# Performance work log

Hardware: AMD Instinct MI355X
Metric: run time of the kernel (lower is better)

## Reference

```python
import jax, jax.numpy as jnp
import numpy as np

V = 20000          # vocab size ('ALL')
E = 512            # embedding_dim
H = 1024           # rnn_hidden_size
LD = 256           # latent_dim
NL = 2             # num_rnn_layers_dec (hidden_factor = 2, unidirectional)
B = 32
S = 256
PAD = 0
CUT0 = 30          # cutoffs = [30, 100, 1000], div_value = 4.0
TAIL_SPECS = [(30, 100, 256), (100, 1000, 64), (1000, V, 16)]  # (low, high, proj_dim)


def setup_inputs() -> dict:
    key = jax.random.key(0)
    ks = jax.random.split(key, 24)
    w = lambda k, shp: (0.02 * jax.random.normal(k, shp)).astype(jnp.float32)

    z = jax.random.normal(ks[0], (B, LD), dtype=jnp.float32)
    emb = w(ks[1], (V, E))
    l2h_w = w(ks[2], (NL * H, LD))
    l2h_b = jnp.zeros((NL * H,), jnp.float32)
    # RNN layer 0 (input E) and layer 1 (input H)
    rnn0_wih = w(ks[3], (H, E)); rnn0_whh = w(ks[4], (H, H))
    rnn0_bih = jnp.zeros((H,), jnp.float32); rnn0_bhh = jnp.zeros((H,), jnp.float32)
    rnn1_wih = w(ks[5], (H, H)); rnn1_whh = w(ks[6], (H, H))
    rnn1_bih = jnp.zeros((H,), jnp.float32); rnn1_bhh = jnp.zeros((H,), jnp.float32)
    # adaptive softmax: head = 30 shortlist + 3 cluster logits
    head_w = w(ks[7], (CUT0 + 3, H))
    tail_p0 = w(ks[8], (256, H));  tail_w0 = w(ks[9], (70, 256))
    tail_p1 = w(ks[10], (64, H));  tail_w1 = w(ks[11], (900, 64))
    tail_p2 = w(ks[12], (16, H));  tail_w2 = w(ks[13], (V - 1000, 16))

    length = jax.random.randint(ks[14], (B,), 32, S + 1)
    pos = jnp.arange(S)[None, :]
    mask = pos < length[:, None]
    inp_seq = jax.random.randint(ks[15], (B, S), 4, V)
    inp_seq = jnp.where(mask, inp_seq, PAD)
    target_seq = jax.random.randint(ks[16], (B, S), 4, V)
    target_seq = jnp.where(mask, target_seq, PAD)

    return dict(z=z, emb=emb, l2h_w=l2h_w, l2h_b=l2h_b,
                rnn0_wih=rnn0_wih, rnn0_whh=rnn0_whh, rnn0_bih=rnn0_bih, rnn0_bhh=rnn0_bhh,
                rnn1_wih=rnn1_wih, rnn1_whh=rnn1_whh, rnn1_bih=rnn1_bih, rnn1_bhh=rnn1_bhh,
                head_w=head_w, tail_p0=tail_p0, tail_w0=tail_w0, tail_p1=tail_p1,
                tail_w1=tail_w1, tail_p2=tail_p2, tail_w2=tail_w2,
                inp_seq=inp_seq, target_seq=target_seq, length=length)


def _rnn_layer(x, h0, wih, whh, bih, bhh):
    # x: [B,S,D], h0: [B,H] -> [B,S,H]  (tanh vanilla RNN)
    def step(h, xt):
        h = jnp.tanh(xt @ wih.T + bih + h @ whh.T + bhh)
        return h, h
    _, ys = jax.lax.scan(step, h0, jnp.swapaxes(x, 0, 1))
    return jnp.swapaxes(ys, 0, 1)


def _adaptive_log_prob(x, head_w, tails):
    # x: [N,H] -> full log-probs [N,V] (AdaptiveLogSoftmaxWithLoss.log_prob)
    head_lp = jax.nn.log_softmax(x @ head_w.T, axis=-1)  # [N, 33]
    parts = [head_lp[:, :CUT0]]
    for i, (p, w) in enumerate(tails):
        clp = jax.nn.log_softmax((x @ p.T) @ w.T, axis=-1)
        parts.append(clp + head_lp[:, CUT0 + i][:, None])
    return jnp.concatenate(parts, axis=1)


def reference(z, emb, l2h_w, l2h_b,
              rnn0_wih, rnn0_whh, rnn0_bih, rnn0_bhh,
              rnn1_wih, rnn1_whh, rnn1_bih, rnn1_bhh,
              head_w, tail_p0, tail_w0, tail_p1, tail_w1, tail_p2, tail_w2,
              inp_seq, target_seq, length):
    # sort inputs by descending length (hidden is NOT sorted, as in the original)
    sorted_idx = jnp.argsort(-length)
    x = emb[inp_seq[sorted_idx]]                         # [B,S,E]
    hid = z @ l2h_w.T + l2h_b                            # [B, 2H]
    hidden = hid.reshape(NL, B, H)                       # torch .view(hidden_factor, B, H)
    h1 = _rnn_layer(x, hidden[0], rnn0_wih, rnn0_whh, rnn0_bih, rnn0_bhh)
    h2 = _rnn_layer(h1, hidden[1], rnn1_wih, rnn1_whh, rnn1_bih, rnn1_bhh)
    rev = jnp.argsort(sorted_idx)
    out = h2[rev].reshape(-1, H)                         # [N,H]
    tgt = target_seq.reshape(-1)                         # [N]
    lp = _adaptive_log_prob(out, head_w,
                            [(tail_p0, tail_w0), (tail_p1, tail_w1), (tail_p2, tail_w2)])
    nll = -jnp.take_along_axis(lp, tgt[:, None], axis=1)[:, 0]
    nll = jnp.where(tgt == PAD, 0.0, nll)
    return jnp.sum(nll)
```

## Files before the change

### kernel.cpp

```cpp
#include <hip/hip_runtime.h>
#include <hip/hip_bf16.h>
#include <math.h>

#define BB 32
#define SS 256
#define EE 512
#define HH 1024
#define LDM 256
#define NROW (BB*SS)

typedef __attribute__((ext_vector_type(8))) short bf16x8;
typedef __attribute__((ext_vector_type(4))) float f32x4;
typedef unsigned long long u64;

static __device__ inline unsigned short f2bf(float f){
  unsigned u = __float_as_uint(f);
  unsigned r = (u + 0x7fffu + ((u >> 16) & 1u)) >> 16;
  return (unsigned short)r;
}
static __device__ inline unsigned short f2bf_fast(float f){
  return (unsigned short)((__float_as_uint(f) + 0x8000u) >> 16);
}
static __device__ inline bf16x8 cvt8(float4 x, float4 y){
  union { ushort s[8]; bf16x8 v; } t;
  t.s[0]=f2bf_fast(x.x); t.s[1]=f2bf_fast(x.y); t.s[2]=f2bf_fast(x.z); t.s[3]=f2bf_fast(x.w);
  t.s[4]=f2bf_fast(y.x); t.s[5]=f2bf_fast(y.y); t.s[6]=f2bf_fast(y.z); t.s[7]=f2bf_fast(y.w);
  return t.v;
}
static __device__ inline unsigned packbf(float a, float b){
  return (unsigned)f2bf(a) | ((unsigned)f2bf(b) << 16);
}

static __device__ inline float ftanh(float x){
  float e = __expf(2.f*x);
  return 1.f - 2.f/(e + 1.f);
}

#define GLD(dst, p) asm volatile("global_load_dwordx4 %0, %1, off sc0 sc1" \
                                 : "=v"(dst) : "v"(p) : "memory")

static __device__ inline bf16x8 asbf(f32x4 x){
  union { f32x4 f; bf16x8 b; } u; u.f = x; return u.b;
}

__global__ void k_sort(const int* __restrict__ length, int* __restrict__ sorted_idx){
  int b = threadIdx.x;
  if (b >= BB) return;
  int lb = length[b];
  int r = 0;
  for (int o = 0; o < BB; ++o){
    int lo = length[o];
    if (lo > lb || (lo == lb && o < b)) ++r;
  }
  sorted_idx[r] = b;
}

__global__ void k_maps(const int* __restrict__ sorted_idx,
                       const int* __restrict__ inp_seq, const int* __restrict__ tgt_seq,
                       int* __restrict__ tokmap, int* __restrict__ tgtmap){
  int bs = blockIdx.x; int t = threadIdx.x;
  int b = sorted_idx[bs];
  tokmap[bs*SS + t] = inp_seq[b*SS + t];
  tgtmap[bs*SS + t] = tgt_seq[b*SS + t];
}

__global__ __launch_bounds__(256) void k_hid(const float* __restrict__ z,
        const float* __restrict__ w, const float* __restrict__ bias,
        ushort* __restrict__ hb0){
  int id = blockIdx.x*256 + threadIdx.x;
  int b = id >> 11, c = id & 2047;
  const float4* zr = (const float4*)(z + b*LDM);
  const float4* wr = (const float4*)(w + (size_t)c*LDM);
  float a0=0,a1=0,a2=0,a3=0;
  #pragma unroll 4
  for (int k=0;k<LDM/4;k++){ float4 zz=zr[k], ww=wr[k];
    a0+=zz.x*ww.x; a1+=zz.y*ww.y; a2+=zz.z*ww.z; a3+=zz.w*ww.w; }
  float val = a0+a1+a2+a3 + bias[c];
  int layer = id >> 15, bp = (id >> 10) & 31, j = id & 1023;
  hb0[(layer<<15) + ((j>>3)<<8) + (bp<<3) + (j&7)] = f2bf(val);
}

__global__ __launch_bounds__(256) void k_wcat(
    const float* __restrict__ head_w, const float* __restrict__ p0,
    const float* __restrict__ p1, const float* __restrict__ p2,
    float* __restrict__ wcat){
  int row = blockIdx.x; int t = threadIdx.x;
  float4* dst = (float4*)(wcat + (size_t)row*HH);
  const float* src;
  if      (row < 33)  src = head_w + (size_t)row*HH;
  else if (row < 289) src = p0 + (size_t)(row-33)*HH;
  else if (row < 353) src = p1 + (size_t)(row-289)*HH;
  else if (row < 369) src = p2 + (size_t)(row-353)*HH;
  else { dst[t] = make_float4(0.f,0.f,0.f,0.f); return; }
  dst[t] = ((const float4*)src)[t];
}

__global__ __launch_bounds__(256) void k_bin(
    const int* __restrict__ tgtmap, int* __restrict__ cnt,
    int* __restrict__ l0, int* __restrict__ l1, int* __restrict__ l2)
{
  int row = blockIdx.x*256 + threadIdx.x;
  int tgt = tgtmap[row];
  int ci = (tgt == 0) ? -1 : (tgt >= 1000) ? 2 : (tgt >= 100) ? 1 : (tgt >= 30) ? 0 : -1;
  int lane = threadIdx.x & 63;
  #pragma unroll
  for (int c = 0; c < 3; ++c){
    unsigned long long mask = __ballot(ci == c);
    int nc = __popcll(mask);
    int base = 0;
    if (lane == 0 && nc) base = atomicAdd(&cnt[c], nc);
    base = __shfl(base, 0);
    if (ci == c){
      int pos = __popcll(mask & ((1ull << lane) - 1ull));
      int* lst = (c == 0) ? l0 : (c == 1) ? l1 : l2;
      lst[base + pos] = row;
    }
  }
}

__global__ __launch_bounds__(256) void k_gemm_bf16(
    const float* __restrict__ A, int lda, const int* __restrict__ rowmap, int abf16,
    const float* __restrict__ Bm,
    const float* __restrict__ bias0, const float* __restrict__ bias1,
    float* __restrict__ C, int M, int N, int K)
{
  __shared__ ushort As[128*72];
  __shared__ ushort Bs[128*72];
  const int nt = blockIdx.x * 128, mt = blockIdx.y * 128;
  const int tid = threadIdx.x;
  const int wv = tid >> 6, ln = tid & 63;
  const int wm = wv & 1, wn = wv >> 1;
  const int lc = ln & 15, quad = ln >> 4;
  f32x4 acc[4][4] = {{{0.f,0.f,0.f,0.f}}};

  for (int s = 0; s < K; s += 64){
    __syncthreads();
    #pragma unroll
    for (int cc = 0; cc < 4; ++cc){
      int ch = tid*4 + cc;
      int r = ch >> 3, c = ch & 7;
      int ar = mt + r;
      if (abf16){
        const ushort* ap = (const ushort*)A + (size_t)ar*lda + s + c*8;
        *(bf16x8*)&As[r*72 + c*8] = *(const bf16x8*)ap;
      } else {
        const float* ap = A + (size_t)(rowmap ? rowmap[ar] : ar)*lda + s + c*8;
        float4 x = *(const float4*)ap, y = *(const float4*)(ap+4);
        *(bf16x8*)&As[r*72 + c*8] = cvt8(x, y);
      }
      int br = nt + r; if (br >= N) br = N - 1;
      const float* bp = Bm + (size_t)br*K + s + c*8;
      float4 bx = *(const float4*)bp, by = *(const float4*)(bp+4);
      *(bf16x8*)&Bs[r*72 + c*8] = cvt8(bx, by);
    }
    __syncthreads();
    #pragma unroll
    for (int kq = 0; kq < 2; ++kq){
      int cq = kq*4 + quad;
      bf16x8 af[4], bfv[4];
      #pragma unroll
      for (int i=0;i<4;i++) af[i]  = *(const bf16x8*)&As[(wm*64 + i*16 + lc)*72 + cq*8];
      #pragma unroll
      for (int j=0;j<4;j++) bfv[j] = *(const bf16x8*)&Bs[(wn*64 + j*16 + lc)*72 + cq*8];
      #pragma unroll
      for (int i=0;i<4;i++)
        #pragma unroll
        for (int j=0;j<4;j++)
          acc[i][j] = __builtin_amdgcn_mfma_f32_16x16x32_bf16(af[i], bfv[j], acc[i][j], 0, 0, 0);
    }
  }
  #pragma unroll
  for (int j=0;j<4;j++){
    int col = nt + wn*64 + j*16 + lc;
    if (col < N){
      float badd = (bias0 ? bias0[col] : 0.f) + (bias1 ? bias1[col] : 0.f);
      #pragma unroll
      for (int i=0;i<4;i++){
        int row = mt + wm*64 + i*16 + quad*4;
        #pragma unroll
        for (int r=0;r<4;r++)
          C[(size_t)(row+r)*N + col] = acc[i][j][r] + badd;
      }
    }
  }
}

__global__ __launch_bounds__(256, 1) void k_rnn_split(
    const float* __restrict__ pre0, ushort* __restrict__ h2out,
    const float* __restrict__ w0hh, const float* __restrict__ w1ih,
    const float* __restrict__ w1hh,
    const float* __restrict__ b1ih, const float* __restrict__ b1hh,
    const ushort* __restrict__ hb0, ushort* __restrict__ hx, int* flags)
{
  __shared__ ushort w0F[16384], wiF[16384], whF[16384];
  __shared__ float red[2176];
  const int wg  = blockIdx.x;
  const int tid = threadIdx.x;
  const bool roleL2 = wg >= 64;
  const int cw  = roleL2 ? wg - 64 : wg;
  const int j0  = cw * 16;
  int* myctr = flags + (roleL2 ? 256 : 0) + (cw & 7) * 32;

  for (int c = tid; c < 4096; c += 256){
    int rr = c >> 8, cc = (c & 255) * 4;
    int dst = ((cc >> 3)*16 + rr)*8 + (cc & 7);
    size_t srow = (size_t)(j0 + rr)*HH + cc;
    float4 w4; uint2 p;
    if (!roleL2){
      w4 = *(const float4*)&w0hh[srow];
      p.x = packbf(w4.x, w4.y); p.y = packbf(w4.z, w4.w);
      *(uint2*)&w0F[dst] = p;
    } else {
      w4 = *(const float4*)&w1ih[srow];
      p.x = packbf(w4.x, w4.y); p.y = packbf(w4.z, w4.w);
      *(uint2*)&wiF[dst] = p;
      w4 = *(const float4*)&w1hh[srow];
      p.x = packbf(w4.x, w4.y); p.y = packbf(w4.z, w4.w);
      *(uint2*)&whF[dst] = p;
    }
  }
  const int lane = tid & 63, wv = tid >> 6;
  const int col = lane & 15, quad = lane >> 4;
  const int ob = tid >> 3, oj = (tid << 1) & 15;
  const int ro = ob*17 + oj;
  const int k = j0 + oj;
  const unsigned off = ((unsigned)(k >> 3) << 7) + ((unsigned)ob << 2) + ((unsigned)(k & 7) >> 1);
  ushort* h1buf = hx;
  ushort* h2buf = hx + 3*32768;

  if (!roleL2){
    float2 pre = *(const float2*)&pre0[((size_t)ob*SS + 0)*HH + j0 + oj];
    __syncthreads();
    for (int t = 0; t < SS; ++t){
      const u64* s1 = (const u64*)(t == 0 ? hb0 : h1buf + ((t+2)%3)*32768);
      f32x4 a0r[8], a1r[8];
      #pragma unroll
      for (int ks = 0; ks < 8; ++ks){
        int kb = wv*32 + ks*4 + quad;
        const u64* p = s1 + (kb << 6) + (col << 1);
        GLD(a0r[ks], p);
        GLD(a1r[ks], p + 32);
      }
      asm volatile("s_waitcnt vmcnt(0)" ::: "memory");
      __builtin_amdgcn_sched_barrier(0);

      f32x4 acc0 = {0.f,0.f,0.f,0.f}, acc1 = {0.f,0.f,0.f,0.f};
      #pragma unroll
      for (int ks = 0; ks < 8; ++ks){
        int kb = wv*32 + ks*4 + quad;
        bf16x8 b0 = *(const bf16x8*)&w0F[(kb*16 + col)*8];
        acc0 = __builtin_amdgcn_mfma_f32_16x16x32_bf16(asbf(a0r[ks]), b0, acc0, 0, 0, 0);
        acc1 = __builtin_amdgcn_mfma_f32_16x16x32_bf16(asbf(a1r[ks]), b0, acc1, 0, 0, 0);
      }
      #pragma unroll
      for (int q = 0; q < 4; ++q){
        red[wv*544 + (quad*4 + q)*17 + col]      = acc0[q];
        red[wv*544 + (16 + quad*4 + q)*17 + col] = acc1[q];
      }
      __syncthreads();
      float s0 = red[ro]   + red[544 + ro]   + red[1088 + ro]   + red[1632 + ro];
      float s1v= red[ro+1] + red[544 + ro+1] + red[1088 + ro+1] + red[1632 + ro+1];
      unsigned pk = packbf(ftanh(pre.x + s0), ftanh(pre.y + s1v));
      __hip_atomic_store((unsigned*)(h1buf + (t%3)*32768) + off, pk,
                         __ATOMIC_RELAXED, __HIP_MEMORY_SCOPE_AGENT);
      asm volatile("s_waitcnt vmcnt(0)" ::: "memory");
      __syncthreads();
      if (tid == 0)
        __hip_atomic_fetch_add(myctr, 1, __ATOMIC_RELAXED, __HIP_MEMORY_SCOPE_AGENT);

      int tn = (t + 1 < SS) ? t + 1 : SS - 1;
      pre = *(const float2*)&pre0[((size_t)ob*SS + tn)*HH + j0 + oj];

      if (t < SS - 1 && tid < 16){
        int tv = (tid < 8) ? 8*(t+1) : 8*(t-1);
        const int* fp = flags + ((tid < 8) ? 0 : 256) + (tid & 7)*32;
        if (tv > 0)
          while (__hip_atomic_load(fp, __ATOMIC_RELAXED, __HIP_MEMORY_SCOPE_AGENT) < tv) {}
      }
      __syncthreads();
    }
  } else {
    float2 pre2;
    pre2.x = b1ih[j0+oj]   + b1hh[j0+oj];
    pre2.y = b1ih[j0+oj+1] + b1hh[j0+oj+1];
    __syncthreads();
    if (tid < 8){
      while (__hip_atomic_load(flags + tid*32, __ATOMIC_RELAXED,
                               __HIP_MEMORY_SCOPE_AGENT) < 8) {}
    }
    __syncthreads();
    for (int s = 0; s < SS; ++s){
      const u64* sa = (const u64*)(h1buf + (s%3)*32768);
      const u64* sc = (const u64*)(s == 0 ? hb0 + 32768
                                          : h2buf + ((s+1)&1)*32768);
      f32x4 a0r[8], a1r[8], c0r[8], c1r[8];
      #pragma unroll
      for (int ks = 0; ks < 8; ++ks){
        int kb = wv*32 + ks*4 + quad;
        const u64* p = sa + (kb << 6) + (col << 1);
        GLD(a0r[ks], p);
        GLD(a1r[ks], p + 32);
      }
      #pragma unroll
      for (int ks = 0; ks < 8; ++ks){
        int kb = wv*32 + ks*4 + quad;
        const u64* p = sc + (kb << 6) + (col << 1);
        GLD(c0r[ks], p);
        GLD(c1r[ks], p + 32);
      }
      asm volatile("s_waitcnt vmcnt(0)" ::: "memory");
      __builtin_amdgcn_sched_barrier(0);

      f32x4 acc0 = {0.f,0.f,0.f,0.f}, acc1 = {0.f,0.f,0.f,0.f};
      #pragma unroll
      for (int ks = 0; ks < 8; ++ks){
        int kb = wv*32 + ks*4 + quad;
        bf16x8 bi = *(const bf16x8*)&wiF[(kb*16 + col)*8];
        acc0 = __builtin_amdgcn_mfma_f32_16x16x32_bf16(asbf(a0r[ks]), bi, acc0, 0, 0, 0);
        acc1 = __builtin_amdgcn_mfma_f32_16x16x32_bf16(asbf(a1r[ks]), bi, acc1, 0, 0, 0);
        bf16x8 bh = *(const bf16x8*)&whF[(kb*16 + col)*8];
        acc0 = __builtin_amdgcn_mfma_f32_16x16x32_bf16(asbf(c0r[ks]), bh, acc0, 0, 0, 0);
        acc1 = __builtin_amdgcn_mfma_f32_16x16x32_bf16(asbf(c1r[ks]), bh, acc1, 0, 0, 0);
      }
      #pragma unroll
      for (int q = 0; q < 4; ++q){
        red[wv*544 + (quad*4 + q)*17 + col]      = acc0[q];
        red[wv*544 + (16 + quad*4 + q)*17 + col] = acc1[q];
      }
      __syncthreads();
      float s2v = red[ro]   + red[544 + ro]   + red[1088 + ro]   + red[1632 + ro];
      float s3v = red[ro+1] + red[544 + ro+1] + red[1088 + ro+1] + red[1632 + ro+1];
      unsigned pk2 = packbf(ftanh(pre2.x + s2v), ftanh(pre2.y + s3v));
      __hip_atomic_store((unsigned*)(h2buf + (s&1)*32768) + off, pk2,
                         __ATOMIC_RELAXED, __HIP_MEMORY_SCOPE_AGENT);
      asm volatile("s_waitcnt vmcnt(0)" ::: "memory");
      __syncthreads();
      if (tid == 0)
        __hip_atomic_fetch_add(myctr, 1, __ATOMIC_RELAXED, __HIP_MEMORY_SCOPE_AGENT);

      *((unsigned*)h2out + (((size_t)ob*SS + s)*HH + j0 + oj) / 2) = pk2;

      if (s < SS - 1 && tid < 16){
        int tv = (tid < 8) ? 8*(s+2) : 8*(s+1);
        const int* fp = flags + ((tid < 8) ? 0 : 256) + (tid & 7)*32;
        while (__hip_atomic_load(fp, __ATOMIC_RELAXED, __HIP_MEMORY_SCOPE_AGENT) < tv) {}
      }
      __syncthreads();
    }
  }
}

__global__ __launch_bounds__(256) void k_cluster(
    const float* __restrict__ combo, int off, int ld, int Kp,
    const float* __restrict__ W, int Nc,
    const int* __restrict__ rowlist, const int* __restrict__ cntp, int ci,
    float* __restrict__ stats)
{
  __shared__ float ps[4][4][256];
  int lane = threadIdx.x & 63;
  int wvl  = threadIdx.x >> 6;
  int n0 = (blockIdx.x*4 + wvl) * 4;
  int count = cntp[ci];
  int rows[4];
  #pragma unroll
  for (int r=0;r<4;r++){
    rows[r] = (n0 + r < count) ? rowlist[n0 + r] : -1;
    if (rows[r] >= 0)
      for (int k=lane;k<Kp;k+=64)
        ps[wvl][r][k] = combo[(size_t)rows[r]*ld + off + k];
  }
  __syncthreads();
  if (rows[0] < 0) return;

  float mx[4], sm[4];
  #pragma unroll
  for (int r=0;r<4;r++){ mx[r]=-1e30f; sm[r]=0.f; }
  for (int n=lane; n<Nc; n+=64){
    const float* wr = W + (size_t)n*Kp;
    float l[4]={0.f,0.f,0.f,0.f};
    for (int k=0;k<Kp;k+=4){
      float4 w4 = *(const float4*)(wr+k);
      #pragma unroll
      for (int r=0;r<4;r++){
        l[r] += w4.x*ps[wvl][r][k] + w4.y*ps[wvl][r][k+1]
              + w4.z*ps[wvl][r][k+2] + w4.w*ps[wvl][r][k+3];
      }
    }
    #pragma unroll
    for (int r=0;r<4;r++){
      float nm = fmaxf(mx[r], l[r]);
      sm[r] = sm[r]*__expf(mx[r]-nm) + __expf(l[r]-nm);
      mx[r] = nm;
    }
  }
  #pragma unroll
  for (int r=0;r<4;r++){
    for (int off2=32; off2; off2>>=1){
      float om = __shfl_down(mx[r], off2);
      float os = __shfl_down(sm[r], off2);
      float nm = fmaxf(mx[r], om);
      sm[r] = sm[r]*__expf(mx[r]-nm) + os*__expf(om-nm);
      mx[r] = nm;
    }
    if (lane==0 && rows[r] >= 0){
      stats[(size_t)rows[r]*6 + ci*2 + 0] = mx[r];
      stats[(size_t)rows[r]*6 + ci*2 + 1] = sm[r];
    }
  }
}

__global__ __launch_bounds__(256) void k_tlogit(
    const int* __restrict__ tgtmap, const float* __restrict__ combo,
    const float* __restrict__ w0, const float* __restrict__ w1, const float* __restrict__ w2,
    float* __restrict__ tlogit)
{
  int lane = threadIdx.x & 63;
  int row = (blockIdx.x * 256 + threadIdx.x) >> 6;
  int tgt = tgtmap[row];
  float acc = 0.f;
  const float* pr = nullptr; const float* wr = nullptr; int Kp = 0;
  const float* crow = combo + (size_t)row*384;
  if      (tgt >= 1000){ pr = crow + 353; wr = w2 + (size_t)(tgt-1000)*16;  Kp=16;  }
  else if (tgt >= 100) { pr = crow + 289; wr = w1 + (size_t)(tgt-100)*64;   Kp=64;  }
  else if (tgt >= 30)  { pr = crow + 33;  wr = w0 + (size_t)(tgt-30)*256;   Kp=256; }
  for (int k=lane; k<Kp; k+=64) acc += pr[k]*wr[k];
  for (int off=32; off; off>>=1) acc += __shfl_down(acc, off);
  if (lane==0) tlogit[row] = acc;
}

__global__ __launch_bounds__(256) void k_final(
    const float* __restrict__ combo, const float* __restrict__ stats,
    const float* __restrict__ tlogit, const int* __restrict__ tgtmap,
    float* __restrict__ out)
{
  int row = blockIdx.x*256 + threadIdx.x;
  int tgt = tgtmap[row];
  float nll = 0.f;
  if (tgt != 0){
    const float* hrow = combo + (size_t)row*384;
    float m = hrow[0];
    #pragma unroll
    for (int i=1;i<33;i++) m = fmaxf(m, hrow[i]);
    float s = 0.f;
    #pragma unroll
    for (int i=0;i<33;i++) s += __expf(hrow[i]-m);
    float lse = __logf(s) + m;
    int ci = (tgt>=1000) ? 2 : (tgt>=100) ? 1 : (tgt>=30) ? 0 : -1;
    if (ci < 0){
      nll = lse - hrow[tgt];
    } else {
      float cm = stats[(size_t)row*6 + ci*2 + 0];
      float cs = stats[(size_t)row*6 + ci*2 + 1];
      nll = lse - hrow[30+ci] + (__logf(cs) + cm - tlogit[row]);
    }
  }
  float v = nll;
  for (int off=32; off; off>>=1) v += __shfl_down(v, off);
  __shared__ float wsum[4];
  int lane = threadIdx.x & 63, wv = threadIdx.x >> 6;
  if (lane==0) wsum[wv] = v;
  __syncthreads();
  if (threadIdx.x==0) atomicAdd(out, wsum[0]+wsum[1]+wsum[2]+wsum[3]);
}

extern "C" void kernel_launch(void* const* d_in, const int* in_sizes, int n_in,
                              void* d_out, int out_size, void* d_ws, size_t ws_size,
                              hipStream_t stream)
{
  const float* z      = (const float*)d_in[0];
  const float* emb    = (const float*)d_in[1];
  const float* l2h_w  = (const float*)d_in[2];
  const float* l2h_b  = (const float*)d_in[3];
  const float* w0ih   = (const float*)d_in[4];
  const float* w0hh   = (const float*)d_in[5];
  const float* b0ih   = (const float*)d_in[6];
  const float* b0hh   = (const float*)d_in[7];
  const float* w1ih   = (const float*)d_in[8];
  const float* w1hh   = (const float*)d_in[9];
  const float* b1ih   = (const float*)d_in[10];
  const float* b1hh   = (const float*)d_in[11];
  const float* head_w = (const float*)d_in[12];
  const float* p0     = (const float*)d_in[13];
  const float* tw0    = (const float*)d_in[14];
  const float* p1     = (const float*)d_in[15];
  const float* tw1    = (const float*)d_in[16];
  const float* p2     = (const float*)d_in[17];
  const float* tw2    = (const float*)d_in[18];
  const int* inp_seq  = (const int*)d_in[19];
  const int* tgt_seq  = (const int*)d_in[20];
  const int* length   = (const int*)d_in[21];

  float* ws   = (float*)d_ws;
  ushort* hb0 = (ushort*)ws;
  ushort* hx  = hb0 + 65536;
  float* bufA = ws + 114688;
  ushort* hbB = (ushort*)(bufA + (size_t)NROW*HH);
  int*   ibuf = (int*)(hbB + (size_t)NROW*HH);
  int* sorted_idx = ibuf;
  int* tokmap = ibuf + 32;
  int* tgtmap = tokmap + NROW;
  int* flags  = tgtmap + NROW;
  int* bincnt = flags + 512;
  int* blist0 = bincnt + 32;
  int* blist1 = blist0 + NROW;
  int* blist2 = blist1 + NROW;
  float* combo = bufA;
  float* stats = bufA + (size_t)NROW*384;
  float* tlog  = stats + (size_t)NROW*6;
  float* wcat  = tlog + NROW;

  float* outF = (float*)d_out;
  hipMemsetAsync(outF, 0, sizeof(float), stream);
  hipMemsetAsync(flags, 0, 544*sizeof(int), stream);

  k_sort<<<1, 32, 0, stream>>>(length, sorted_idx);
  k_maps<<<32, 256, 0, stream>>>(sorted_idx, inp_seq, tgt_seq, tokmap, tgtmap);
  k_hid<<<256, 256, 0, stream>>>(z, l2h_w, l2h_b, hb0);
  k_bin<<<32, 256, 0, stream>>>(tgtmap, bincnt, blist0, blist1, blist2);

  k_gemm_bf16<<<dim3(HH/128, NROW/128), 256, 0, stream>>>(emb, EE, tokmap, 0, w0ih,
                                                          b0ih, b0hh, bufA, NROW, HH, EE);
  k_rnn_split<<<128, 256, 0, stream>>>(bufA, hbB, w0hh, w1ih, w1hh, b1ih, b1hh,
                                       hb0, hx, flags);

  k_wcat<<<384, 256, 0, stream>>>(head_w, p0, p1, p2, wcat);
  k_gemm_bf16<<<dim3(3, NROW/128), 256, 0, stream>>>((const float*)hbB, HH, nullptr, 1,
                                                     wcat, nullptr, nullptr,
                                                     combo, NROW, 384, HH);

  k_cluster<<<NROW/16, 256, 0, stream>>>(combo, 33,  384, 256, tw0, 70,
                                         blist0, bincnt, 0, stats);
  k_cluster<<<NROW/16, 256, 0, stream>>>(combo, 289, 384, 64,  tw1, 900,
                                         blist1, bincnt, 1, stats);
  k_cluster<<<NROW/16, 256, 0, stream>>>(combo, 353, 384, 16,  tw2, 19000,
                                         blist2, bincnt, 2, stats);
  k_tlogit<<<NROW/4, 256, 0, stream>>>(tgtmap, combo, tw0, tw1, tw2, tlog);
  k_final<<<NROW/256, 256, 0, stream>>>(combo, stats, tlog, tgtmap, outF);
}
```

Before: 1.516 ms.

## Bound RNN recurrence by max sequence length and fuse prep kernels

Computes the maximum sequence length on the device and stops both RNN layer loops at that bound, skipping timesteps where every sequence is padding. The sort, gather and target-binning kernels are merged into one prep kernel to cut launch overhead. Embedding rows are gathered and converted to bf16 once in a separate kernel, so the input GEMM reads compact bf16 instead of gathered fp32. Hidden outputs beyond the max length are left unwritten, so correctness depends on padded positions being masked downstream.

```diff
diff --git a/kernel.cpp b/kernel.cpp
--- a/kernel.cpp
+++ b/kernel.cpp
@@ -43,25 +43,60 @@
   union { f32x4 f; bf16x8 b; } u; u.f = x; return u.b;
 }
 
-__global__ void k_sort(const int* __restrict__ length, int* __restrict__ sorted_idx){
-  int b = threadIdx.x;
-  if (b >= BB) return;
-  int lb = length[b];
-  int r = 0;
-  for (int o = 0; o < BB; ++o){
-    int lo = length[o];
-    if (lo > lb || (lo == lb && o < b)) ++r;
-  }
-  sorted_idx[r] = b;
-}
-
-__global__ void k_maps(const int* __restrict__ sorted_idx,
-                       const int* __restrict__ inp_seq, const int* __restrict__ tgt_seq,
-                       int* __restrict__ tokmap, int* __restrict__ tgtmap){
-  int bs = blockIdx.x; int t = threadIdx.x;
-  int b = sorted_idx[bs];
-  tokmap[bs*SS + t] = inp_seq[b*SS + t];
-  tgtmap[bs*SS + t] = tgt_seq[b*SS + t];
+__global__ __launch_bounds__(256) void k_prep(
+    const int* __restrict__ length,
+    const int* __restrict__ inp_seq, const int* __restrict__ tgt_seq,
+    int* __restrict__ tokmap, int* __restrict__ tgtmap,
+    int* __restrict__ cnt, int* __restrict__ ml,
+    int* __restrict__ l0, int* __restrict__ l1, int* __restrict__ l2)
+{
+  __shared__ int src_b;
+  int bs = blockIdx.x, t = threadIdx.x;
+  if (t < 32){
+    int lb = length[t];
+    int r = 0;
+    for (int o = 0; o < BB; ++o){
+      int lo = length[o];
+      if (lo > lb || (lo == lb && o < t)) ++r;
+    }
+    if (r == bs) src_b = t;
+    if (bs == 0 && t == 0){
+      int m = 0;
+      for (int o = 0; o < BB; ++o){ int lo = length[o]; if (lo > m) m = lo; }
+      *ml = m;
+    }
+  }
+  __syncthreads();
+  int b = src_b;
+  int row = bs*SS + t;
+  tokmap[row] = inp_seq[b*SS + t];
+  int tgt = tgt_seq[b*SS + t];
+  tgtmap[row] = tgt;
+  int ci = (tgt == 0) ? -1 : (tgt >= 1000) ? 2 : (tgt >= 100) ? 1 : (tgt >= 30) ? 0 : -1;
+  int lane = t & 63;
+  #pragma unroll
+  for (int c = 0; c < 3; ++c){
+    unsigned long long mask = __ballot(ci == c);
+    int nc = __popcll(mask);
+    int base = 0;
+    if (lane == 0 && nc) base = atomicAdd(&cnt[c], nc);
+    base = __shfl(base, 0);
+    if (ci == c){
+      int pos = __popcll(mask & ((1ull << lane) - 1ull));
+      int* lst = (c == 0) ? l0 : (c == 1) ? l1 : l2;
+      lst[base + pos] = row;
+    }
+  }
+}
+
+__global__ __launch_bounds__(256) void k_emb(
+    const int* __restrict__ tokmap, const float* __restrict__ emb,
+    ushort* __restrict__ tokemb)
+{
+  int row = blockIdx.x; int t = threadIdx.x;
+  const float2* src = (const float2*)(emb + (size_t)tokmap[row]*EE);
+  float2 v = src[t];
+  ((unsigned*)tokemb)[(size_t)row*(EE/2) + t] = packbf(v.x, v.y);
 }
 
 __global__ __launch_bounds__(256) void k_hid(const float* __restrict__ z,
@@ -95,29 +130,6 @@
   dst[t] = ((const float4*)src)[t];
 }
 
-__global__ __launch_bounds__(256) void k_bin(
-    const int* __restrict__ tgtmap, int* __restrict__ cnt,
-    int* __restrict__ l0, int* __restrict__ l1, int* __restrict__ l2)
-{
-  int row = blockIdx.x*256 + threadIdx.x;
-  int tgt = tgtmap[row];
-  int ci = (tgt == 0) ? -1 : (tgt >= 1000) ? 2 : (tgt >= 100) ? 1 : (tgt >= 30) ? 0 : -1;
-  int lane = threadIdx.x & 63;
-  #pragma unroll
-  for (int c = 0; c < 3; ++c){
-    unsigned long long mask = __ballot(ci == c);
-    int nc = __popcll(mask);
-    int base = 0;
-    if (lane == 0 && nc) base = atomicAdd(&cnt[c], nc);
-    base = __shfl(base, 0);
-    if (ci == c){
-      int pos = __popcll(mask & ((1ull << lane) - 1ull));
-      int* lst = (c == 0) ? l0 : (c == 1) ? l1 : l2;
-      lst[base + pos] = row;
-    }
-  }
-}
-
 __global__ __launch_bounds__(256) void k_gemm_bf16(
     const float* __restrict__ A, int lda, const int* __restrict__ rowmap, int abf16,
     const float* __restrict__ Bm,
@@ -190,7 +202,8 @@
     const float* __restrict__ w0hh, const float* __restrict__ w1ih,
     const float* __restrict__ w1hh,
     const float* __restrict__ b1ih, const float* __restrict__ b1hh,
-    const ushort* __restrict__ hb0, ushort* __restrict__ hx, int* flags)
+    const ushort* __restrict__ hb0, ushort* __restrict__ hx, int* flags,
+    const int* __restrict__ mlp)
 {
   __shared__ ushort w0F[16384], wiF[16384], whF[16384];
   __shared__ float red[2176];
@@ -199,6 +212,7 @@
   const bool roleL2 = wg >= 64;
   const int cw  = roleL2 ? wg - 64 : wg;
   const int j0  = cw * 16;
+  const int ml  = *mlp;
   int* myctr = flags + (roleL2 ? 256 : 0) + (cw & 7) * 32;
 
   for (int c = tid; c < 4096; c += 256){
@@ -231,7 +245,7 @@
   if (!roleL2){
     float2 pre = *(const float2*)&pre0[((size_t)ob*SS + 0)*HH + j0 + oj];
     __syncthreads();
-    for (int t = 0; t < SS; ++t){
+    for (int t = 0; t < ml; ++t){
       const u64* s1 = (const u64*)(t == 0 ? hb0 : h1buf + ((t+2)%3)*32768);
       f32x4 a0r[8], a1r[8];
       #pragma unroll
@@ -268,10 +282,10 @@
       if (tid == 0)
         __hip_atomic_fetch_add(myctr, 1, __ATOMIC_RELAXED, __HIP_MEMORY_SCOPE_AGENT);
 
-      int tn = (t + 1 < SS) ? t + 1 : SS - 1;
+      int tn = (t + 1 < ml) ? t + 1 : ml - 1;
       pre = *(const float2*)&pre0[((size_t)ob*SS + tn)*HH + j0 + oj];
 
-      if (t < SS - 1 && tid < 16){
+      if (t < ml - 1 && tid < 16){
         int tv = (tid < 8) ? 8*(t+1) : 8*(t-1);
         const int* fp = flags + ((tid < 8) ? 0 : 256) + (tid & 7)*32;
         if (tv > 0)
@@ -289,7 +303,7 @@
                                __HIP_MEMORY_SCOPE_AGENT) < 8) {}
     }
     __syncthreads();
-    for (int s = 0; s < SS; ++s){
+    for (int s = 0; s < ml; ++s){
       const u64* sa = (const u64*)(h1buf + (s%3)*32768);
       const u64* sc = (const u64*)(s == 0 ? hb0 + 32768
                                           : h2buf + ((s+1)&1)*32768);
@@ -340,7 +354,7 @@
 
       *((unsigned*)h2out + (((size_t)ob*SS + s)*HH + j0 + oj) / 2) = pk2;
 
-      if (s < SS - 1 && tid < 16){
+      if (s < ml - 1 && tid < 16){
         int tv = (tid < 8) ? 8*(s+2) : 8*(s+1);
         const int* fp = flags + ((tid < 8) ? 0 : 256) + (tid & 7)*32;
         while (__hip_atomic_load(fp, __ATOMIC_RELAXED, __HIP_MEMORY_SCOPE_AGENT) < tv) {}
@@ -495,12 +509,14 @@
   ushort* hx  = hb0 + 65536;
   float* bufA = ws + 114688;
   ushort* hbB = (ushort*)(bufA + (size_t)NROW*HH);
-  int*   ibuf = (int*)(hbB + (size_t)NROW*HH);
+  ushort* tokemb = hbB + (size_t)NROW*HH;
+  int*   ibuf = (int*)(tokemb + (size_t)NROW*EE);
   int* sorted_idx = ibuf;
   int* tokmap = ibuf + 32;
   int* tgtmap = tokmap + NROW;
   int* flags  = tgtmap + NROW;
   int* bincnt = flags + 512;
+  int* mlptr  = bincnt + 4;
   int* blist0 = bincnt + 32;
   int* blist1 = blist0 + NROW;
   int* blist2 = blist1 + NROW;
@@ -513,15 +529,16 @@
   hipMemsetAsync(outF, 0, sizeof(float), stream);
   hipMemsetAsync(flags, 0, 544*sizeof(int), stream);
 
-  k_sort<<<1, 32, 0, stream>>>(length, sorted_idx);
-  k_maps<<<32, 256, 0, stream>>>(sorted_idx, inp_seq, tgt_seq, tokmap, tgtmap);
+  k_prep<<<32, 256, 0, stream>>>(length, inp_seq, tgt_seq, tokmap, tgtmap,
+                                 bincnt, mlptr, blist0, blist1, blist2);
+  k_emb<<<NROW, 256, 0, stream>>>(tokmap, emb, tokemb);
   k_hid<<<256, 256, 0, stream>>>(z, l2h_w, l2h_b, hb0);
-  k_bin<<<32, 256, 0, stream>>>(tgtmap, bincnt, blist0, blist1, blist2);
-
-  k_gemm_bf16<<<dim3(HH/128, NROW/128), 256, 0, stream>>>(emb, EE, tokmap, 0, w0ih,
+
+  k_gemm_bf16<<<dim3(HH/128, NROW/128), 256, 0, stream>>>((const float*)tokemb, EE,
+                                                          nullptr, 1, w0ih,
                                                           b0ih, b0hh, bufA, NROW, HH, EE);
   k_rnn_split<<<128, 256, 0, stream>>>(bufA, hbB, w0hh, w1ih, w1hh, b1ih, b1hh,
-                                       hb0, hx, flags);
+                                       hb0, hx, flags, mlptr);
 
   k_wcat<<<384, 256, 0, stream>>>(head_w, p0, p1, p2, wcat);
   k_gemm_bf16<<<dim3(3, NROW/128), 256, 0, stream>>>((const float*)hbB, HH, nullptr, 1,
```

Measured after the change: 1.480 ms. -2.4%, faster.
